# Performance work log

Hardware: AMD Instinct MI355X
Metric: run time of the kernel (lower is better)

Reference implementation:

```python
import jax, jax.numpy as jnp
import numpy as np

N_NODES = 50000
N_EDGES = 800000
HIDDEN = 128
N_GRAPHS = 256
N_CLASSES = 10


def setup_inputs() -> dict:
    key = jax.random.key(0)
    ks = jax.random.split(key, 9)
    x = jax.random.normal(ks[0], (N_NODES, HIDDEN), dtype=jnp.float32)
    edge_index = jax.random.randint(ks[1], (2, N_EDGES), 0, N_NODES, dtype=jnp.int64)
    batch = jnp.sort(jax.random.randint(ks[2], (N_NODES,), 0, N_GRAPHS, dtype=jnp.int64))
    s = 1.0 / np.sqrt(HIDDEN)
    W1 = jax.random.uniform(ks[3], (HIDDEN, HIDDEN), jnp.float32, -s, s)
    b1 = jax.random.uniform(ks[4], (HIDDEN,), jnp.float32, -s, s)
    W2 = jax.random.uniform(ks[5], (HIDDEN, HIDDEN), jnp.float32, -s, s)
    b2 = jax.random.uniform(ks[6], (HIDDEN,), jnp.float32, -s, s)
    Wl = jax.random.uniform(ks[7], (HIDDEN, N_CLASSES), jnp.float32, -s, s)
    bl = jax.random.uniform(ks[8], (N_CLASSES,), jnp.float32, -s, s)
    return {"x": x, "edge_index": edge_index, "batch": batch,
            "W1": W1, "b1": b1, "W2": W2, "b2": b2, "Wl": Wl, "bl": bl}


def _gin_conv(x, src, dst, W1, b1, W2, b2):
    # GINConv, eps=0: nn(x + sum_{j->i} x_j); messages flow src -> dst
    agg = jax.ops.segment_sum(x[src], dst, num_segments=N_NODES)
    h = x + agg
    h = jnp.maximum(h @ W1 + b1, 0.0) @ W2 + b2  # shared 2-layer MLP
    return h


def reference(x, edge_index, batch, W1, b1, W2, b2, Wl, bl):
    src, dst = edge_index[0], edge_index[1]
    h = jnp.maximum(_gin_conv(x, src, dst, W1, b1, W2, b2), 0.0)
    h = jnp.maximum(_gin_conv(h, src, dst, W1, b1, W2, b2), 0.0)
    h = _gin_conv(h, src, dst, W1, b1, W2, b2)
    # global mean pool over graphs
    sums = jax.ops.segment_sum(h, batch, num_segments=N_GRAPHS)
    cnt = jax.ops.segment_sum(jnp.ones((N_NODES,), h.dtype), batch, num_segments=N_GRAPHS)
    pooled = sums / jnp.maximum(cnt, 1.0)[:, None]
    # dropout is identity in eval mode
    return pooled @ Wl + bl
```

## Files before the change

### kernel.cpp

```cpp
#include <hip/hip_runtime.h>

#define N_NODES  50000
#define N_EDGES  800000
#define HIDDEN   128
#define N_GRAPHS 256
#define N_CLASSES 10
#define WLD 136
#define ZLD 136
#define E_HALF 400000
#define POISON 0xAAAAAAAAu

typedef short short8 __attribute__((ext_vector_type(8)));
typedef float floatx4 __attribute__((ext_vector_type(4)));

__device__ inline unsigned short bf16_rtne(float x) {
    unsigned u = __float_as_uint(x);
    unsigned r = ((u >> 16) & 1u) + 0x7fffu;
    return (unsigned short)((u + r) >> 16);
}

__device__ inline int lower_bound_batch(const int* __restrict__ batch, int target) {
    int lo = 0, hi = N_NODES;
    while (lo < hi) {
        int mid = (lo + hi) >> 1;
        if (batch[mid] < target) lo = mid + 1; else hi = mid;
    }
    return lo;
}

__global__ void prep_kernel(const int* __restrict__ dst, int* __restrict__ deg0, int* __restrict__ deg1,
                            int* __restrict__ epos,
                            const float* __restrict__ W1, unsigned short* __restrict__ W1b,
                            const float* __restrict__ W2, unsigned short* __restrict__ W2b,
                            const float4* __restrict__ X, uint4* __restrict__ Xb,
                            int* __restrict__ counter) {
    int b = blockIdx.x;
    if (b < 3125) {
        int e = b * 256 + threadIdx.x;
        int* degp = (e < E_HALF) ? deg0 : deg1;
        int old = atomicAdd(&degp[dst[e]], 1);
        epos[e] = (int)((unsigned)old - POISON);
    } else if (b < 3253) {
        int idx = (b - 3125) * 256 + threadIdx.x;
        if (idx == 0) counter[0] = 0;
        int which = idx >> 14, sub = idx & (HIDDEN * HIDDEN - 1);
        int k = sub >> 7, n = sub & 127;
        (which ? W2b : W1b)[n * HIDDEN + k] = bf16_rtne((which ? W2 : W1)[sub]);
    } else {
        int i = (b - 3253) * 256 + threadIdx.x;
        int n = i >> 4, c = i & 15;
        float4 a = X[(size_t)n * 32 + c * 2], v = X[(size_t)n * 32 + c * 2 + 1];
        uint4 o;
        o.x = (unsigned)bf16_rtne(a.x) | ((unsigned)bf16_rtne(a.y) << 16);
        o.y = (unsigned)bf16_rtne(a.z) | ((unsigned)bf16_rtne(a.w) << 16);
        o.z = (unsigned)bf16_rtne(v.x) | ((unsigned)bf16_rtne(v.y) << 16);
        o.w = (unsigned)bf16_rtne(v.z) | ((unsigned)bf16_rtne(v.w) << 16);
        Xb[(size_t)(c >> 2) * N_NODES * 4 + (size_t)n * 4 + (c & 3)] = o;
    }
}

__global__ void offsets_kernel(int* __restrict__ deg0, int* __restrict__ deg1,
                               int* __restrict__ row_start, int* __restrict__ counter) {
    int n = blockIdx.x * blockDim.x + threadIdx.x;
    int d0 = 0, dT = 0;
    if (n < N_NODES) {
        d0 = (int)((unsigned)deg0[n] - POISON);
        int d1 = (int)((unsigned)deg1[n] - POISON);
        dT = d0 + d1;
    }
    int lane = threadIdx.x & 63;
    int incl = dT;
    #pragma unroll
    for (int o = 1; o < 64; o <<= 1) {
        int v = __shfl_up(incl, o, 64);
        if (lane >= o) incl += v;
    }
    int excl = incl - dT;
    int total = __shfl(incl, 63, 64);
    int base = 0;
    if (lane == 0) base = atomicAdd(counter, total);
    base = __shfl(base, 0, 64);
    if (n < N_NODES) {
        row_start[n] = base + excl;
        deg0[n] = d0;
        deg1[n] = dT;
    }
}

__global__ void place_kernel(const int* __restrict__ src, const int* __restrict__ dst,
                             const int* __restrict__ epos, const int* __restrict__ row_start,
                             const int* __restrict__ deg0, int* __restrict__ csr_src) {
    int e = blockIdx.x * blockDim.x + threadIdx.x;
    if (e >= N_EDGES) return;
    int d = dst[e];
    int pos = row_start[d] + epos[e];
    if (e >= E_HALF) pos += deg0[d];
    csr_src[pos] = src[e];
}

__device__ inline void acc_bf2(unsigned d, float& f0, float& f1) {
    f0 += __uint_as_float(d << 16);
    f1 += __uint_as_float(d & 0xffff0000u);
}
__device__ inline void acc8(const uint4 v, float* a) {
    acc_bf2(v.x, a[0], a[1]); acc_bf2(v.y, a[2], a[3]);
    acc_bf2(v.z, a[4], a[5]); acc_bf2(v.w, a[6], a[7]);
}

__global__ void agg_kernel(const uint4* __restrict__ Xb, const int* __restrict__ row_start,
                           const int* __restrict__ deg, const int* __restrict__ csr_src,
                           uint4* __restrict__ Tb ) {
    int s = blockIdx.x & 3;
    int n = (blockIdx.x >> 2) * 64 + (threadIdx.x >> 2);
    int chunk = threadIdx.x & 3;
    if (n >= N_NODES) return;
    const uint4* Ts = Xb + (size_t)s * (N_NODES * 4);
    float a[8];
    #pragma unroll
    for (int j = 0; j < 8; ++j) a[j] = 0.f;
    {
        uint4 v = Ts[(size_t)n * 4 + chunk];
        acc8(v, a);
    }
    int rs = row_start[n], d = deg[n];
    int i = 0;
    for (; i + 4 <= d; i += 4) {
        int s0 = csr_src[rs + i + 0];
        int s1 = csr_src[rs + i + 1];
        int s2 = csr_src[rs + i + 2];
        int s3 = csr_src[rs + i + 3];
        uint4 v0 = Ts[(size_t)s0 * 4 + chunk];
        uint4 v1 = Ts[(size_t)s1 * 4 + chunk];
        uint4 v2 = Ts[(size_t)s2 * 4 + chunk];
        uint4 v3 = Ts[(size_t)s3 * 4 + chunk];
        acc8(v0, a); acc8(v1, a); acc8(v2, a); acc8(v3, a);
    }
    for (; i < d; ++i) {
        int s0 = csr_src[rs + i];
        uint4 v0 = Ts[(size_t)s0 * 4 + chunk];
        acc8(v0, a);
    }
    uint4 o;
    o.x = (unsigned)bf16_rtne(a[0]) | ((unsigned)bf16_rtne(a[1]) << 16);
    o.y = (unsigned)bf16_rtne(a[2]) | ((unsigned)bf16_rtne(a[3]) << 16);
    o.z = (unsigned)bf16_rtne(a[4]) | ((unsigned)bf16_rtne(a[5]) << 16);
    o.w = (unsigned)bf16_rtne(a[6]) | ((unsigned)bf16_rtne(a[7]) << 16);
    Tb[(size_t)n * 16 + s * 4 + chunk] = o;
}

__global__ __launch_bounds__(256)
void mlp2_kernel(const unsigned short* __restrict__ Ab,
                 const unsigned short* __restrict__ W1b,
                 const float* __restrict__ b1,
                 const unsigned short* __restrict__ W2b,
                 const float* __restrict__ b2,
                 unsigned short* __restrict__ Cb, int relu2, int blocked,
                 const int* __restrict__ batch, float* __restrict__ pooled, int pool_mode) {
    __shared__ unsigned short W2S[HIDDEN * WLD];
    __shared__ unsigned short zS[128 * ZLD];

    int t = threadIdx.x;
    {
        const short8* gh = (const short8*)W2b;
        #pragma unroll
        for (int i = 0; i < 8; ++i) {
            int idx = i * 256 + t;
            int row = idx >> 4, kk = (idx & 15) * 8;
            *(short8*)(W2S + row * WLD + kk) = gh[idx];
        }
    }
    __syncthreads();

    int w = t >> 6, l = t & 63;
    int lane16 = l & 15, quad = l >> 4;
    int node_base = blockIdx.x * 128;

    floatx4 acc[2][8];
    #pragma unroll
    for (int m = 0; m < 2; ++m)
        #pragma unroll
        for (int nt = 0; nt < 8; ++nt) acc[m][nt] = (floatx4){0.f, 0.f, 0.f, 0.f};

    #pragma unroll
    for (int kc = 0; kc < 4; ++kc) {
        int k0 = kc * 32 + quad * 8;
        short8 bt[8];
        #pragma unroll
        for (int nt = 0; nt < 8; ++nt) {
            int r = node_base + nt * 16 + lane16;
            if (r < N_NODES) bt[nt] = *(const short8*)(Ab + (size_t)r * HIDDEN + k0);
            else             bt[nt] = (short8){0,0,0,0,0,0,0,0};
        }
        short8 aw[2];
        #pragma unroll
        for (int m = 0; m < 2; ++m) {
            int zc = (2 * w + m) * 16 + lane16;
            aw[m] = *(const short8*)(W1b + (size_t)zc * HIDDEN + k0);
        }
        #pragma unroll
        for (int m = 0; m < 2; ++m)
            #pragma unroll
            for (int nt = 0; nt < 8; ++nt)
                acc[m][nt] = __builtin_amdgcn_mfma_f32_16x16x32_bf16(aw[m], bt[nt], acc[m][nt], 0, 0, 0);
    }
    #pragma unroll
    for (int m = 0; m < 2; ++m) {
        int zc0 = (2 * w + m) * 16 + quad * 4;
        float4 bb = *(const float4*)(b1 + zc0);
        #pragma unroll
        for (int nt = 0; nt < 8; ++nt) {
            int node = nt * 16 + lane16;
            ushort4 pk;
            pk.x = bf16_rtne(fmaxf(acc[m][nt][0] + bb.x, 0.f));
            pk.y = bf16_rtne(fmaxf(acc[m][nt][1] + bb.y, 0.f));
            pk.z = bf16_rtne(fmaxf(acc[m][nt][2] + bb.z, 0.f));
            pk.w = bf16_rtne(fmaxf(acc[m][nt][3] + bb.w, 0.f));
            *(ushort4*)(zS + node * ZLD + zc0) = pk;
        }
    }
    __syncthreads();

    floatx4 acc2[2][8];
    #pragma unroll
    for (int m = 0; m < 2; ++m)
        #pragma unroll
        for (int nt = 0; nt < 8; ++nt) acc2[m][nt] = (floatx4){0.f, 0.f, 0.f, 0.f};

    #pragma unroll
    for (int kc = 0; kc < 4; ++kc) {
        int k0 = kc * 32 + quad * 8;
        short8 az[2];
        #pragma unroll
        for (int m = 0; m < 2; ++m) {
            int lr = w * 32 + m * 16 + lane16;
            az[m] = *(const short8*)(zS + lr * ZLD + k0);
        }
        short8 bh[8];
        #pragma unroll
        for (int nt = 0; nt < 8; ++nt)
            bh[nt] = *(const short8*)(W2S + (nt * 16 + lane16) * WLD + k0);
        #pragma unroll
        for (int m = 0; m < 2; ++m)
            #pragma unroll
            for (int nt = 0; nt < 8; ++nt)
                acc2[m][nt] = __builtin_amdgcn_mfma_f32_16x16x32_bf16(az[m], bh[nt], acc2[m][nt], 0, 0, 0);
    }

    if (!pool_mode) {
        #pragma unroll
        for (int nt = 0; nt < 8; ++nt) {
            int col = nt * 16 + lane16;
            float b = b2[col];
            #pragma unroll
            for (int m = 0; m < 2; ++m) {
                #pragma unroll
                for (int reg = 0; reg < 4; ++reg) {
                    int r = node_base + w * 32 + m * 16 + quad * 4 + reg;
                    if (r < N_NODES) {
                        float o = acc2[m][nt][reg] + b;
                        if (relu2) o = fmaxf(o, 0.f);
                        size_t oi = blocked
                            ? ((size_t)(col >> 5) * N_NODES + r) * 32 + (col & 31)
                            : (size_t)r * HIDDEN + col;
                        Cb[oi] = bf16_rtne(o);
                    }
                }
            }
        }
        return;
    }

    __syncthreads();
    #pragma unroll
    for (int nt = 0; nt < 8; ++nt) {
        int col = nt * 16 + lane16;
        float b = b2[col];
        #pragma unroll
        for (int m = 0; m < 2; ++m) {
            #pragma unroll
            for (int reg = 0; reg < 4; ++reg) {
                int rl = w * 32 + m * 16 + quad * 4 + reg;
                float o = acc2[m][nt][reg] + b;
                zS[rl * ZLD + col] = bf16_rtne(o);
            }
        }
    }
    __syncthreads();

    int row_end = min(node_base + 128, N_NODES);
    int g0 = batch[node_base];
    int gend = batch[row_end - 1];
    int c = t & 127, half = t >> 7;
    for (int g = g0; g <= gend; ++g) {
        int lo = (g == g0)   ? node_base : lower_bound_batch(batch, g);
        int hi = (g == gend) ? row_end   : lower_bound_batch(batch, g + 1);
        if (lo < node_base) lo = node_base;
        if (hi > row_end)   hi = row_end;
        float s = 0.f;
        for (int r = lo + half; r < hi; r += 2)
            s += __uint_as_float((unsigned)zS[(r - node_base) * ZLD + c] << 16);
        if (hi > lo) atomicAdd(&pooled[(size_t)g * HIDDEN + c], s);
    }
}

__global__ void head_kernel(const float* __restrict__ pooled, const int* __restrict__ batch,
                            const float* __restrict__ Wl, const float* __restrict__ bl,
                            float* __restrict__ out) {
    int g = blockIdx.x;
    int t = threadIdx.x;
    __shared__ int bounds[2];
    __shared__ float mean[HIDDEN];
    if (t < 2) bounds[t] = lower_bound_batch(batch, g + t);
    __syncthreads();
    float cntf = (float)(bounds[1] - bounds[0]);
    mean[t] = pooled[(size_t)g * HIDDEN + t] / fmaxf(cntf, 1.0f);
    __syncthreads();
    if (t < N_CLASSES) {
        float o = bl[t];
        #pragma unroll 8
        for (int k = 0; k < HIDDEN; ++k) o = fmaf(mean[k], Wl[k * N_CLASSES + t], o);
        out[(size_t)g * N_CLASSES + t] = o;
    }
}

extern "C" void kernel_launch(void* const* d_in, const int* in_sizes, int n_in,
                              void* d_out, int out_size, void* d_ws, size_t ws_size,
                              hipStream_t stream) {
    const float* x   = (const float*)d_in[0];
    const int*   ei  = (const int*)d_in[1];
    const int*   bat = (const int*)d_in[2];
    const float* W1  = (const float*)d_in[3];
    const float* b1  = (const float*)d_in[4];
    const float* W2  = (const float*)d_in[5];
    const float* b2  = (const float*)d_in[6];
    const float* Wl  = (const float*)d_in[7];
    const float* bl  = (const float*)d_in[8];
    float* out = (float*)d_out;

    const int* src = ei;
    const int* dst = ei + N_EDGES;

    char* w = (char*)d_ws;
    size_t off = 0;
    auto alloc = [&](size_t bytes) { void* p = w + off; off = (off + bytes + 255) & ~(size_t)255; return p; };
    unsigned short* g_bf  = (unsigned short*)alloc((size_t)N_NODES * HIDDEN * 2);
    unsigned short* t_bf  = (unsigned short*)alloc((size_t)N_NODES * HIDDEN * 2);
    float* pooled  = (float*)alloc((size_t)N_GRAPHS * HIDDEN * 4);
    int*   deg0    = (int*)  alloc((size_t)N_NODES * 4);
    int*   deg1    = (int*)  alloc((size_t)N_NODES * 4);
    int*   rowst   = (int*)  alloc((size_t)N_NODES * 4);
    int*   epos    = (int*)  alloc((size_t)N_EDGES * 4);
    int*   csr_src = (int*)  alloc((size_t)N_EDGES * 4);
    int*   counter = (int*)  alloc(256);
    unsigned short* w1b = (unsigned short*)alloc((size_t)HIDDEN * HIDDEN * 2);
    unsigned short* w2b = (unsigned short*)alloc((size_t)HIDDEN * HIDDEN * 2);
    (void)ws_size; (void)in_sizes; (void)n_in; (void)out_size;

    prep_kernel<<<6378, 256, 0, stream>>>(dst, deg0, deg1, epos, W1, w1b, W2, w2b,
                                          (const float4*)x, (uint4*)g_bf, counter);
    offsets_kernel<<<(N_NODES + 255) / 256, 256, 0, stream>>>(deg0, deg1, rowst, counter);
    place_kernel<<<(N_EDGES + 255) / 256, 256, 0, stream>>>(src, dst, epos, rowst, deg0, csr_src);

    const int agg_grid = 4 * ((N_NODES + 63) / 64);
    const int mlp_grid = (N_NODES + 127) / 128;
    unsigned short* nus = (unsigned short*)nullptr;

    agg_kernel<<<agg_grid, 256, 0, stream>>>((const uint4*)g_bf, rowst, deg1, csr_src, (uint4*)t_bf);
    mlp2_kernel<<<mlp_grid, 256, 0, stream>>>(t_bf, w1b, b1, w2b, b2, g_bf, 1, 1, bat, (float*)nullptr, 0);
    agg_kernel<<<agg_grid, 256, 0, stream>>>((const uint4*)g_bf, rowst, deg1, csr_src, (uint4*)t_bf);
    mlp2_kernel<<<mlp_grid, 256, 0, stream>>>(t_bf, w1b, b1, w2b, b2, g_bf, 1, 1, bat, (float*)nullptr, 0);
    agg_kernel<<<agg_grid, 256, 0, stream>>>((const uint4*)g_bf, rowst, deg1, csr_src, (uint4*)t_bf);
    mlp2_kernel<<<mlp_grid, 256, 0, stream>>>(t_bf, w1b, b1, w2b, b2, nus, 0, 0, bat, pooled, 1);

    head_kernel<<<N_GRAPHS, HIDDEN, 0, stream>>>(pooled, bat, Wl, bl, out);
}
```

Before: 317.1 us.

## Fuse neighbor aggregation into the GIN MLP kernel via shared memory

Merges the separate aggregation kernel into the MLP kernel: each block gathers neighbor sums for its 128 nodes straight into the shared z buffer, then runs both MFMA GEMMs from shared memory. It also drops the feature-blocked layout in favour of row-major bf16 storage, so each gather reads a full 256-byte row per node. This removes the intermediate aggregate round trip through global memory and three kernel launches. In exchange, the gather now runs with only 391 blocks, which lowers the parallelism available to hide latency, and the per-block gather work is uneven across nodes with different degrees.

```diff
diff --git a/kernel.cpp b/kernel.cpp
--- a/kernel.cpp
+++ b/kernel.cpp
@@ -55,7 +55,7 @@
         o.y = (unsigned)bf16_rtne(a.z) | ((unsigned)bf16_rtne(a.w) << 16);
         o.z = (unsigned)bf16_rtne(v.x) | ((unsigned)bf16_rtne(v.y) << 16);
         o.w = (unsigned)bf16_rtne(v.z) | ((unsigned)bf16_rtne(v.w) << 16);
-        Xb[(size_t)(c >> 2) * N_NODES * 4 + (size_t)n * 4 + (c & 3)] = o;
+        Xb[(size_t)n * 16 + c] = o;
     }
 }
 
@@ -107,55 +107,14 @@
     acc_bf2(v.z, a[4], a[5]); acc_bf2(v.w, a[6], a[7]);
 }
 
-__global__ void agg_kernel(const uint4* __restrict__ Xb, const int* __restrict__ row_start,
-                           const int* __restrict__ deg, const int* __restrict__ csr_src,
-                           uint4* __restrict__ Tb ) {
-    int s = blockIdx.x & 3;
-    int n = (blockIdx.x >> 2) * 64 + (threadIdx.x >> 2);
-    int chunk = threadIdx.x & 3;
-    if (n >= N_NODES) return;
-    const uint4* Ts = Xb + (size_t)s * (N_NODES * 4);
-    float a[8];
-    #pragma unroll
-    for (int j = 0; j < 8; ++j) a[j] = 0.f;
-    {
-        uint4 v = Ts[(size_t)n * 4 + chunk];
-        acc8(v, a);
-    }
-    int rs = row_start[n], d = deg[n];
-    int i = 0;
-    for (; i + 4 <= d; i += 4) {
-        int s0 = csr_src[rs + i + 0];
-        int s1 = csr_src[rs + i + 1];
-        int s2 = csr_src[rs + i + 2];
-        int s3 = csr_src[rs + i + 3];
-        uint4 v0 = Ts[(size_t)s0 * 4 + chunk];
-        uint4 v1 = Ts[(size_t)s1 * 4 + chunk];
-        uint4 v2 = Ts[(size_t)s2 * 4 + chunk];
-        uint4 v3 = Ts[(size_t)s3 * 4 + chunk];
-        acc8(v0, a); acc8(v1, a); acc8(v2, a); acc8(v3, a);
-    }
-    for (; i < d; ++i) {
-        int s0 = csr_src[rs + i];
-        uint4 v0 = Ts[(size_t)s0 * 4 + chunk];
-        acc8(v0, a);
-    }
-    uint4 o;
-    o.x = (unsigned)bf16_rtne(a[0]) | ((unsigned)bf16_rtne(a[1]) << 16);
-    o.y = (unsigned)bf16_rtne(a[2]) | ((unsigned)bf16_rtne(a[3]) << 16);
-    o.z = (unsigned)bf16_rtne(a[4]) | ((unsigned)bf16_rtne(a[5]) << 16);
-    o.w = (unsigned)bf16_rtne(a[6]) | ((unsigned)bf16_rtne(a[7]) << 16);
-    Tb[(size_t)n * 16 + s * 4 + chunk] = o;
-}
-
 __global__ __launch_bounds__(256)
-void mlp2_kernel(const unsigned short* __restrict__ Ab,
-                 const unsigned short* __restrict__ W1b,
-                 const float* __restrict__ b1,
-                 const unsigned short* __restrict__ W2b,
-                 const float* __restrict__ b2,
-                 unsigned short* __restrict__ Cb, int relu2, int blocked,
-                 const int* __restrict__ batch, float* __restrict__ pooled, int pool_mode) {
+void fused_gin_layer(const unsigned short* __restrict__ Hin,
+                     const int* __restrict__ row_start, const int* __restrict__ deg,
+                     const int* __restrict__ csr_src,
+                     const unsigned short* __restrict__ W1b, const float* __restrict__ b1,
+                     const unsigned short* __restrict__ W2b, const float* __restrict__ b2,
+                     unsigned short* __restrict__ Hout, int relu2,
+                     const int* __restrict__ batch, float* __restrict__ pooled, int pool_mode) {
     __shared__ unsigned short W2S[HIDDEN * WLD];
     __shared__ unsigned short zS[128 * ZLD];
 
@@ -169,11 +128,52 @@
             *(short8*)(W2S + row * WLD + kk) = gh[idx];
         }
     }
+
+    int node_base = blockIdx.x * 128;
+    const uint4* H4 = (const uint4*)Hin;
+
+    {
+        int c = t & 15;
+        int nl0 = t >> 4;
+        for (int rr = 0; rr < 8; ++rr) {
+            int nl = rr * 16 + nl0;
+            int n = node_base + nl;
+            float a[8];
+            #pragma unroll
+            for (int j = 0; j < 8; ++j) a[j] = 0.f;
+            if (n < N_NODES) {
+                acc8(H4[(size_t)n * 16 + c], a);
+                int rs = row_start[n], d = deg[n];
+                int i = 0;
+                for (; i + 4 <= d; i += 4) {
+                    int s0 = csr_src[rs + i + 0];
+                    int s1 = csr_src[rs + i + 1];
+                    int s2 = csr_src[rs + i + 2];
+                    int s3 = csr_src[rs + i + 3];
+                    uint4 v0 = H4[(size_t)s0 * 16 + c];
+                    uint4 v1 = H4[(size_t)s1 * 16 + c];
+                    uint4 v2 = H4[(size_t)s2 * 16 + c];
+                    uint4 v3 = H4[(size_t)s3 * 16 + c];
+                    acc8(v0, a); acc8(v1, a); acc8(v2, a); acc8(v3, a);
+                }
+                for (; i < d; ++i) {
+                    uint4 v0 = H4[(size_t)csr_src[rs + i] * 16 + c];
+                    acc8(v0, a);
+                }
+            }
+            ushort4 p0, p1;
+            p0.x = bf16_rtne(a[0]); p0.y = bf16_rtne(a[1]);
+            p0.z = bf16_rtne(a[2]); p0.w = bf16_rtne(a[3]);
+            p1.x = bf16_rtne(a[4]); p1.y = bf16_rtne(a[5]);
+            p1.z = bf16_rtne(a[6]); p1.w = bf16_rtne(a[7]);
+            *(ushort4*)(zS + nl * ZLD + c * 8) = p0;
+            *(ushort4*)(zS + nl * ZLD + c * 8 + 4) = p1;
+        }
+    }
     __syncthreads();
 
     int w = t >> 6, l = t & 63;
     int lane16 = l & 15, quad = l >> 4;
-    int node_base = blockIdx.x * 128;
 
     floatx4 acc[2][8];
     #pragma unroll
@@ -186,11 +186,8 @@
         int k0 = kc * 32 + quad * 8;
         short8 bt[8];
         #pragma unroll
-        for (int nt = 0; nt < 8; ++nt) {
-            int r = node_base + nt * 16 + lane16;
-            if (r < N_NODES) bt[nt] = *(const short8*)(Ab + (size_t)r * HIDDEN + k0);
-            else             bt[nt] = (short8){0,0,0,0,0,0,0,0};
-        }
+        for (int nt = 0; nt < 8; ++nt)
+            bt[nt] = *(const short8*)(zS + (nt * 16 + lane16) * ZLD + k0);
         short8 aw[2];
         #pragma unroll
         for (int m = 0; m < 2; ++m) {
@@ -203,6 +200,8 @@
             for (int nt = 0; nt < 8; ++nt)
                 acc[m][nt] = __builtin_amdgcn_mfma_f32_16x16x32_bf16(aw[m], bt[nt], acc[m][nt], 0, 0, 0);
     }
+    __syncthreads();
+
     #pragma unroll
     for (int m = 0; m < 2; ++m) {
         int zc0 = (2 * w + m) * 16 + quad * 4;
@@ -259,10 +258,7 @@
                     if (r < N_NODES) {
                         float o = acc2[m][nt][reg] + b;
                         if (relu2) o = fmaxf(o, 0.f);
-                        size_t oi = blocked
-                            ? ((size_t)(col >> 5) * N_NODES + r) * 32 + (col & 31)
-                            : (size_t)r * HIDDEN + col;
-                        Cb[oi] = bf16_rtne(o);
+                        Hout[(size_t)r * HIDDEN + col] = bf16_rtne(o);
                     }
                 }
             }
@@ -361,16 +357,15 @@
     offsets_kernel<<<(N_NODES + 255) / 256, 256, 0, stream>>>(deg0, deg1, rowst, counter);
     place_kernel<<<(N_EDGES + 255) / 256, 256, 0, stream>>>(src, dst, epos, rowst, deg0, csr_src);
 
-    const int agg_grid = 4 * ((N_NODES + 63) / 64);
-    const int mlp_grid = (N_NODES + 127) / 128;
+    const int grid = (N_NODES + 127) / 128;
     unsigned short* nus = (unsigned short*)nullptr;
 
-    agg_kernel<<<agg_grid, 256, 0, stream>>>((const uint4*)g_bf, rowst, deg1, csr_src, (uint4*)t_bf);
-    mlp2_kernel<<<mlp_grid, 256, 0, stream>>>(t_bf, w1b, b1, w2b, b2, g_bf, 1, 1, bat, (float*)nullptr, 0);
-    agg_kernel<<<agg_grid, 256, 0, stream>>>((const uint4*)g_bf, rowst, deg1, csr_src, (uint4*)t_bf);
-    mlp2_kernel<<<mlp_grid, 256, 0, stream>>>(t_bf, w1b, b1, w2b, b2, g_bf, 1, 1, bat, (float*)nullptr, 0);
-    agg_kernel<<<agg_grid, 256, 0, stream>>>((const uint4*)g_bf, rowst, deg1, csr_src, (uint4*)t_bf);
-    mlp2_kernel<<<mlp_grid, 256, 0, stream>>>(t_bf, w1b, b1, w2b, b2, nus, 0, 0, bat, pooled, 1);
+    fused_gin_layer<<<grid, 256, 0, stream>>>(g_bf, rowst, deg1, csr_src, w1b, b1, w2b, b2,
+                                              t_bf, 1, bat, (float*)nullptr, 0);
+    fused_gin_layer<<<grid, 256, 0, stream>>>(t_bf, rowst, deg1, csr_src, w1b, b1, w2b, b2,
+                                              g_bf, 1, bat, (float*)nullptr, 0);
+    fused_gin_layer<<<grid, 256, 0, stream>>>(g_bf, rowst, deg1, csr_src, w1b, b1, w2b, b2,
+                                              nus, 0, bat, pooled, 1);
 
     head_kernel<<<N_GRAPHS, HIDDEN, 0, stream>>>(pooled, bat, Wl, bl, out);
 }
```

After: 343.7 us. +8.4%, slower.

## Merge CSR preprocessing into one cooperative kernel and halve MLP tile

Applied to the files above, without the earlier changes.

The three preprocessing kernels (degree count plus conversions, offset scan, edge placement) become one cooperative kernel with grid-wide syncs, which removes two kernel launch boundaries. The MLP kernel now handles 64 nodes per block instead of 128, drops the LDS staging of W2 and reads W2 fragments straight from global memory. This doubles the block count to improve occupancy and shrinks LDS use. The costs are grid-sync overhead, repeated global or L2 reads of W2, and halved reuse of the W1 fragments per block.

```diff
diff --git a/kernel.cpp b/kernel.cpp
--- a/kernel.cpp
+++ b/kernel.cpp
@@ -1,11 +1,13 @@
 #include <hip/hip_runtime.h>
+#include <hip/hip_cooperative_groups.h>
+
+namespace cg = cooperative_groups;
 
 #define N_NODES  50000
 #define N_EDGES  800000
 #define HIDDEN   128
 #define N_GRAPHS 256
 #define N_CLASSES 10
-#define WLD 136
 #define ZLD 136
 #define E_HALF 400000
 #define POISON 0xAAAAAAAAu
@@ -28,74 +30,78 @@
     return lo;
 }
 
-__global__ void prep_kernel(const int* __restrict__ dst, int* __restrict__ deg0, int* __restrict__ deg1,
-                            int* __restrict__ epos,
-                            const float* __restrict__ W1, unsigned short* __restrict__ W1b,
-                            const float* __restrict__ W2, unsigned short* __restrict__ W2b,
-                            const float4* __restrict__ X, uint4* __restrict__ Xb,
-                            int* __restrict__ counter) {
-    int b = blockIdx.x;
-    if (b < 3125) {
+__global__ __launch_bounds__(256, 4)
+void prep_all(const int* __restrict__ src, const int* __restrict__ dst,
+              int* __restrict__ deg0, int* __restrict__ deg1,
+              int* __restrict__ epos, int* __restrict__ row_start,
+              int* __restrict__ csr_src, int* __restrict__ counter,
+              const float* __restrict__ W1, unsigned short* __restrict__ W1b,
+              const float* __restrict__ W2, unsigned short* __restrict__ W2b,
+              const float4* __restrict__ X, uint4* __restrict__ Xb) {
+    cg::grid_group gg = cg::this_grid();
+    const int nb = gridDim.x;
+
+    for (int b = blockIdx.x; b < 6378; b += nb) {
+        if (b < 3125) {
+            int e = b * 256 + threadIdx.x;
+            int* degp = (e < E_HALF) ? deg0 : deg1;
+            int old = atomicAdd(&degp[dst[e]], 1);
+            epos[e] = (int)((unsigned)old - POISON);
+        } else if (b < 3253) {
+            int idx = (b - 3125) * 256 + threadIdx.x;
+            if (idx == 0) counter[0] = 0;
+            int which = idx >> 14, sub = idx & (HIDDEN * HIDDEN - 1);
+            int k = sub >> 7, n = sub & 127;
+            (which ? W2b : W1b)[n * HIDDEN + k] = bf16_rtne((which ? W2 : W1)[sub]);
+        } else {
+            int i = (b - 3253) * 256 + threadIdx.x;
+            int n = i >> 4, c = i & 15;
+            float4 a = X[(size_t)n * 32 + c * 2], v = X[(size_t)n * 32 + c * 2 + 1];
+            uint4 o;
+            o.x = (unsigned)bf16_rtne(a.x) | ((unsigned)bf16_rtne(a.y) << 16);
+            o.y = (unsigned)bf16_rtne(a.z) | ((unsigned)bf16_rtne(a.w) << 16);
+            o.z = (unsigned)bf16_rtne(v.x) | ((unsigned)bf16_rtne(v.y) << 16);
+            o.w = (unsigned)bf16_rtne(v.z) | ((unsigned)bf16_rtne(v.w) << 16);
+            Xb[(size_t)(c >> 2) * N_NODES * 4 + (size_t)n * 4 + (c & 3)] = o;
+        }
+    }
+    gg.sync();
+
+    for (int b = blockIdx.x; b < 196; b += nb) {
+        int n = b * 256 + threadIdx.x;
+        int d0 = 0, dT = 0;
+        if (n < N_NODES) {
+            d0 = (int)((unsigned)deg0[n] - POISON);
+            int d1 = (int)((unsigned)deg1[n] - POISON);
+            dT = d0 + d1;
+        }
+        int lane = threadIdx.x & 63;
+        int incl = dT;
+        #pragma unroll
+        for (int o = 1; o < 64; o <<= 1) {
+            int v = __shfl_up(incl, o, 64);
+            if (lane >= o) incl += v;
+        }
+        int excl = incl - dT;
+        int total = __shfl(incl, 63, 64);
+        int base = 0;
+        if (lane == 0) base = atomicAdd(counter, total);
+        base = __shfl(base, 0, 64);
+        if (n < N_NODES) {
+            row_start[n] = base + excl;
+            deg0[n] = d0;
+            deg1[n] = dT;
+        }
+    }
+    gg.sync();
+
+    for (int b = blockIdx.x; b < 3125; b += nb) {
         int e = b * 256 + threadIdx.x;
-        int* degp = (e < E_HALF) ? deg0 : deg1;
-        int old = atomicAdd(&degp[dst[e]], 1);
-        epos[e] = (int)((unsigned)old - POISON);
-    } else if (b < 3253) {
-        int idx = (b - 3125) * 256 + threadIdx.x;
-        if (idx == 0) counter[0] = 0;
-        int which = idx >> 14, sub = idx & (HIDDEN * HIDDEN - 1);
-        int k = sub >> 7, n = sub & 127;
-        (which ? W2b : W1b)[n * HIDDEN + k] = bf16_rtne((which ? W2 : W1)[sub]);
-    } else {
-        int i = (b - 3253) * 256 + threadIdx.x;
-        int n = i >> 4, c = i & 15;
-        float4 a = X[(size_t)n * 32 + c * 2], v = X[(size_t)n * 32 + c * 2 + 1];
-        uint4 o;
-        o.x = (unsigned)bf16_rtne(a.x) | ((unsigned)bf16_rtne(a.y) << 16);
-        o.y = (unsigned)bf16_rtne(a.z) | ((unsigned)bf16_rtne(a.w) << 16);
-        o.z = (unsigned)bf16_rtne(v.x) | ((unsigned)bf16_rtne(v.y) << 16);
-        o.w = (unsigned)bf16_rtne(v.z) | ((unsigned)bf16_rtne(v.w) << 16);
-        Xb[(size_t)(c >> 2) * N_NODES * 4 + (size_t)n * 4 + (c & 3)] = o;
-    }
-}
-
-__global__ void offsets_kernel(int* __restrict__ deg0, int* __restrict__ deg1,
-                               int* __restrict__ row_start, int* __restrict__ counter) {
-    int n = blockIdx.x * blockDim.x + threadIdx.x;
-    int d0 = 0, dT = 0;
-    if (n < N_NODES) {
-        d0 = (int)((unsigned)deg0[n] - POISON);
-        int d1 = (int)((unsigned)deg1[n] - POISON);
-        dT = d0 + d1;
-    }
-    int lane = threadIdx.x & 63;
-    int incl = dT;
-    #pragma unroll
-    for (int o = 1; o < 64; o <<= 1) {
-        int v = __shfl_up(incl, o, 64);
-        if (lane >= o) incl += v;
-    }
-    int excl = incl - dT;
-    int total = __shfl(incl, 63, 64);
-    int base = 0;
-    if (lane == 0) base = atomicAdd(counter, total);
-    base = __shfl(base, 0, 64);
-    if (n < N_NODES) {
-        row_start[n] = base + excl;
-        deg0[n] = d0;
-        deg1[n] = dT;
-    }
-}
-
-__global__ void place_kernel(const int* __restrict__ src, const int* __restrict__ dst,
-                             const int* __restrict__ epos, const int* __restrict__ row_start,
-                             const int* __restrict__ deg0, int* __restrict__ csr_src) {
-    int e = blockIdx.x * blockDim.x + threadIdx.x;
-    if (e >= N_EDGES) return;
-    int d = dst[e];
-    int pos = row_start[d] + epos[e];
-    if (e >= E_HALF) pos += deg0[d];
-    csr_src[pos] = src[e];
+        int d = dst[e];
+        int pos = row_start[d] + epos[e];
+        if (e >= E_HALF) pos += deg0[d];
+        csr_src[pos] = src[e];
+    }
 }
 
 __device__ inline void acc_bf2(unsigned d, float& f0, float& f1) {
@@ -149,44 +155,30 @@
 }
 
 __global__ __launch_bounds__(256)
-void mlp2_kernel(const unsigned short* __restrict__ Ab,
-                 const unsigned short* __restrict__ W1b,
-                 const float* __restrict__ b1,
-                 const unsigned short* __restrict__ W2b,
-                 const float* __restrict__ b2,
-                 unsigned short* __restrict__ Cb, int relu2, int blocked,
-                 const int* __restrict__ batch, float* __restrict__ pooled, int pool_mode) {
-    __shared__ unsigned short W2S[HIDDEN * WLD];
-    __shared__ unsigned short zS[128 * ZLD];
+void mlp64_kernel(const unsigned short* __restrict__ Ab,
+                  const unsigned short* __restrict__ W1b, const float* __restrict__ b1,
+                  const unsigned short* __restrict__ W2b, const float* __restrict__ b2,
+                  unsigned short* __restrict__ Cb, int relu2, int blocked,
+                  const int* __restrict__ batch, float* __restrict__ pooled, int pool_mode) {
+    __shared__ unsigned short zS[64 * ZLD];
 
     int t = threadIdx.x;
-    {
-        const short8* gh = (const short8*)W2b;
-        #pragma unroll
-        for (int i = 0; i < 8; ++i) {
-            int idx = i * 256 + t;
-            int row = idx >> 4, kk = (idx & 15) * 8;
-            *(short8*)(W2S + row * WLD + kk) = gh[idx];
-        }
-    }
-    __syncthreads();
-
     int w = t >> 6, l = t & 63;
     int lane16 = l & 15, quad = l >> 4;
-    int node_base = blockIdx.x * 128;
-
-    floatx4 acc[2][8];
+    int node_base = blockIdx.x * 64;
+
+    floatx4 acc[2][4];
     #pragma unroll
     for (int m = 0; m < 2; ++m)
         #pragma unroll
-        for (int nt = 0; nt < 8; ++nt) acc[m][nt] = (floatx4){0.f, 0.f, 0.f, 0.f};
+        for (int nt = 0; nt < 4; ++nt) acc[m][nt] = (floatx4){0.f, 0.f, 0.f, 0.f};
 
     #pragma unroll
     for (int kc = 0; kc < 4; ++kc) {
         int k0 = kc * 32 + quad * 8;
-        short8 bt[8];
-        #pragma unroll
-        for (int nt = 0; nt < 8; ++nt) {
+        short8 bt[4];
+        #pragma unroll
+        for (int nt = 0; nt < 4; ++nt) {
             int r = node_base + nt * 16 + lane16;
             if (r < N_NODES) bt[nt] = *(const short8*)(Ab + (size_t)r * HIDDEN + k0);
             else             bt[nt] = (short8){0,0,0,0,0,0,0,0};
@@ -200,7 +192,7 @@
         #pragma unroll
         for (int m = 0; m < 2; ++m)
             #pragma unroll
-            for (int nt = 0; nt < 8; ++nt)
+            for (int nt = 0; nt < 4; ++nt)
                 acc[m][nt] = __builtin_amdgcn_mfma_f32_16x16x32_bf16(aw[m], bt[nt], acc[m][nt], 0, 0, 0);
     }
     #pragma unroll
@@ -208,7 +200,7 @@
         int zc0 = (2 * w + m) * 16 + quad * 4;
         float4 bb = *(const float4*)(b1 + zc0);
         #pragma unroll
-        for (int nt = 0; nt < 8; ++nt) {
+        for (int nt = 0; nt < 4; ++nt) {
             int node = nt * 16 + lane16;
             ushort4 pk;
             pk.x = bf16_rtne(fmaxf(acc[m][nt][0] + bb.x, 0.f));
@@ -220,30 +212,21 @@
     }
     __syncthreads();
 
-    floatx4 acc2[2][8];
-    #pragma unroll
-    for (int m = 0; m < 2; ++m)
-        #pragma unroll
-        for (int nt = 0; nt < 8; ++nt) acc2[m][nt] = (floatx4){0.f, 0.f, 0.f, 0.f};
+    floatx4 acc2[8];
+    #pragma unroll
+    for (int nt = 0; nt < 8; ++nt) acc2[nt] = (floatx4){0.f, 0.f, 0.f, 0.f};
 
     #pragma unroll
     for (int kc = 0; kc < 4; ++kc) {
         int k0 = kc * 32 + quad * 8;
-        short8 az[2];
-        #pragma unroll
-        for (int m = 0; m < 2; ++m) {
-            int lr = w * 32 + m * 16 + lane16;
-            az[m] = *(const short8*)(zS + lr * ZLD + k0);
-        }
+        short8 az = *(const short8*)(zS + (w * 16 + lane16) * ZLD + k0);
         short8 bh[8];
         #pragma unroll
         for (int nt = 0; nt < 8; ++nt)
-            bh[nt] = *(const short8*)(W2S + (nt * 16 + lane16) * WLD + k0);
-        #pragma unroll
-        for (int m = 0; m < 2; ++m)
-            #pragma unroll
-            for (int nt = 0; nt < 8; ++nt)
-                acc2[m][nt] = __builtin_amdgcn_mfma_f32_16x16x32_bf16(az[m], bh[nt], acc2[m][nt], 0, 0, 0);
+            bh[nt] = *(const short8*)(W2b + (size_t)(nt * 16 + lane16) * HIDDEN + k0);
+        #pragma unroll
+        for (int nt = 0; nt < 8; ++nt)
+            acc2[nt] = __builtin_amdgcn_mfma_f32_16x16x32_bf16(az, bh[nt], acc2[nt], 0, 0, 0);
     }
 
     if (!pool_mode) {
@@ -252,18 +235,15 @@
             int col = nt * 16 + lane16;
             float b = b2[col];
             #pragma unroll
-            for (int m = 0; m < 2; ++m) {
-                #pragma unroll
-                for (int reg = 0; reg < 4; ++reg) {
-                    int r = node_base + w * 32 + m * 16 + quad * 4 + reg;
-                    if (r < N_NODES) {
-                        float o = acc2[m][nt][reg] + b;
-                        if (relu2) o = fmaxf(o, 0.f);
-                        size_t oi = blocked
-                            ? ((size_t)(col >> 5) * N_NODES + r) * 32 + (col & 31)
-                            : (size_t)r * HIDDEN + col;
-                        Cb[oi] = bf16_rtne(o);
-                    }
+            for (int reg = 0; reg < 4; ++reg) {
+                int r = node_base + w * 16 + quad * 4 + reg;
+                if (r < N_NODES) {
+                    float o = acc2[nt][reg] + b;
+                    if (relu2) o = fmaxf(o, 0.f);
+                    size_t oi = blocked
+                        ? ((size_t)(col >> 5) * N_NODES + r) * 32 + (col & 31)
+                        : (size_t)r * HIDDEN + col;
+                    Cb[oi] = bf16_rtne(o);
                 }
             }
         }
@@ -276,18 +256,15 @@
         int col = nt * 16 + lane16;
         float b = b2[col];
         #pragma unroll
-        for (int m = 0; m < 2; ++m) {
-            #pragma unroll
-            for (int reg = 0; reg < 4; ++reg) {
-                int rl = w * 32 + m * 16 + quad * 4 + reg;
-                float o = acc2[m][nt][reg] + b;
-                zS[rl * ZLD + col] = bf16_rtne(o);
-            }
-        }
-    }
-    __syncthreads();
-
-    int row_end = min(node_base + 128, N_NODES);
+        for (int reg = 0; reg < 4; ++reg) {
+            int rl = w * 16 + quad * 4 + reg;
+            float o = acc2[nt][reg] + b;
+            zS[rl * ZLD + col] = bf16_rtne(o);
+        }
+    }
+    __syncthreads();
+
+    int row_end = min(node_base + 64, N_NODES);
     int g0 = batch[node_base];
     int gend = batch[row_end - 1];
     int c = t & 127, half = t >> 7;
@@ -356,21 +333,28 @@
     unsigned short* w2b = (unsigned short*)alloc((size_t)HIDDEN * HIDDEN * 2);
     (void)ws_size; (void)in_sizes; (void)n_in; (void)out_size;
 
-    prep_kernel<<<6378, 256, 0, stream>>>(dst, deg0, deg1, epos, W1, w1b, W2, w2b,
-                                          (const float4*)x, (uint4*)g_bf, counter);
-    offsets_kernel<<<(N_NODES + 255) / 256, 256, 0, stream>>>(deg0, deg1, rowst, counter);
-    place_kernel<<<(N_EDGES + 255) / 256, 256, 0, stream>>>(src, dst, epos, rowst, deg0, csr_src);
+    {
+        const float4* Xc = (const float4*)x;
+        uint4* Xbv = (uint4*)g_bf;
+        void* args[] = {
+            (void*)&src, (void*)&dst, (void*)&deg0, (void*)&deg1,
+            (void*)&epos, (void*)&rowst, (void*)&csr_src, (void*)&counter,
+            (void*)&W1, (void*)&w1b, (void*)&W2, (void*)&w2b,
+            (void*)&Xc, (void*)&Xbv
+        };
+        hipLaunchCooperativeKernel((void*)prep_all, dim3(1024), dim3(256), args, 0, stream);
+    }
 
     const int agg_grid = 4 * ((N_NODES + 63) / 64);
-    const int mlp_grid = (N_NODES + 127) / 128;
+    const int mlp_grid = (N_NODES + 63) / 64;
     unsigned short* nus = (unsigned short*)nullptr;
 
     agg_kernel<<<agg_grid, 256, 0, stream>>>((const uint4*)g_bf, rowst, deg1, csr_src, (uint4*)t_bf);
-    mlp2_kernel<<<mlp_grid, 256, 0, stream>>>(t_bf, w1b, b1, w2b, b2, g_bf, 1, 1, bat, (float*)nullptr, 0);
+    mlp64_kernel<<<mlp_grid, 256, 0, stream>>>(t_bf, w1b, b1, w2b, b2, g_bf, 1, 1, bat, (float*)nullptr, 0);
     agg_kernel<<<agg_grid, 256, 0, stream>>>((const uint4*)g_bf, rowst, deg1, csr_src, (uint4*)t_bf);
-    mlp2_kernel<<<mlp_grid, 256, 0, stream>>>(t_bf, w1b, b1, w2b, b2, g_bf, 1, 1, bat, (float*)nullptr, 0);
+    mlp64_kernel<<<mlp_grid, 256, 0, stream>>>(t_bf, w1b, b1, w2b, b2, g_bf, 1, 1, bat, (float*)nullptr, 0);
     agg_kernel<<<agg_grid, 256, 0, stream>>>((const uint4*)g_bf, rowst, deg1, csr_src, (uint4*)t_bf);
-    mlp2_kernel<<<mlp_grid, 256, 0, stream>>>(t_bf, w1b, b1, w2b, b2, nus, 0, 0, bat, pooled, 1);
+    mlp64_kernel<<<mlp_grid, 256, 0, stream>>>(t_bf, w1b, b1, w2b, b2, nus, 0, 0, bat, pooled, 1);
 
     head_kernel<<<N_GRAPHS, HIDDEN, 0, stream>>>(pooled, bat, Wl, bl, out);
 }
```

Measured after the change: 562.5 us. 77.4% more time.
